# Optimization experiments

Hardware: AMD Instinct MI355X
Metric: run time of the kernel (lower is better)

The kernel has to match this reference:

```python
import jax, jax.numpy as jnp
import numpy as np

EMBED_DIM = 512

def setup_inputs() -> dict:
    key = jax.random.key(0)
    ks = jax.random.split(key, 8)
    B, N, M, C = 4, 4096, 4096, EMBED_DIM
    s = 1.0 / np.sqrt(C)
    return {
        "rgb_features": jax.random.normal(ks[0], (B, N, C), jnp.float32),
        "depth_features": jax.random.normal(ks[1], (B, M, C), jnp.float32),
        "Wq": jax.random.normal(ks[2], (C, C), jnp.float32) * s,
        "bq": jnp.zeros((C,), jnp.float32),
        "Wk": jax.random.normal(ks[3], (C, C), jnp.float32) * s,
        "bk": jnp.zeros((C,), jnp.float32),
        "Wv": jax.random.normal(ks[4], (C, C), jnp.float32) * s,
        "bv": jnp.zeros((C,), jnp.float32),
    }

def reference(rgb_features, depth_features, Wq, bq, Wk, bk, Wv, bv):
    C = rgb_features.shape[-1]
    scale = C ** (-0.5)
    Q = rgb_features @ Wq + bq          # [B, N, C]
    K = depth_features @ Wk + bk        # [B, M, C]
    V = depth_features @ Wv + bv        # [B, M, C]
    scores = jnp.einsum('bnc,bmc->bnm', Q, K) * scale
    attn = jax.nn.softmax(scores, axis=-1)
    return jnp.einsum('bnm,bmc->bnc', attn, V)
```

## Files before the change

kernel.cpp:

```cpp
#include <hip/hip_runtime.h>
#include <hip/hip_bf16.h>
#include <stdint.h>


typedef unsigned short u16;
typedef __attribute__((ext_vector_type(8))) short bf16x8;
typedef __attribute__((ext_vector_type(16))) float f32x16;
typedef __attribute__((ext_vector_type(4))) unsigned short u16x4;

#define GLD_LDS16(g, l)                                                        \
  __builtin_amdgcn_global_load_lds(                                            \
      (const __attribute__((address_space(1))) unsigned int*)(g),              \
      (__attribute__((address_space(3))) unsigned int*)(l), 16, 0, 0)

__device__ __forceinline__ u16 f2bf(float f) {
  unsigned x = __float_as_uint(f);
  return (u16)((x + 0x7fffu + ((x >> 16) & 1u)) >> 16);
}
__device__ __forceinline__ float bf2f(short s) {
  return __uint_as_float((unsigned)(unsigned short)s << 16);
}

template <int TM, int TN, int WC, int BIAS_MODE, bool OUT_F32, int MINW>
__global__ __launch_bounds__(256, MINW) void gemm32(
    const u16* __restrict__ A, const u16* __restrict__ Bm,
    const float* __restrict__ bias, void* __restrict__ Cv, int M, int N, int K,
    long long sAb, long long sBb, long long sCb) {
  constexpr int WROWS = TM * WC / 4;
  constexpr int WCOLS = TN / WC;
  constexpr int MSUB = WROWS / 32;
  constexpr int NSUB = WCOLS / 32;
  constexpr int CA = TM / 64;
  constexpr int CB = TN / 64;

  const int bz = blockIdx.z;
  A += (size_t)bz * sAb;
  Bm += (size_t)bz * sBb;

  const int bm = blockIdx.y * TM;
  const int bn = blockIdx.x * TN;

  __shared__ u16 As[TM * 32];
  __shared__ u16 Bs[TN * 32];

  const int tid = threadIdx.x;
  const int wave = tid >> 6;
  const int lane = tid & 63;
  const int ln31 = lane & 31;
  const int half = lane >> 5;
  const int wr = wave / WC;
  const int wc = wave % WC;

  const int rowA = lane >> 2;
  const int swz = ((lane & 3) ^ ((rowA + (rowA >> 2)) & 3)) * 8;
  const int gl = (ln31 + (ln31 >> 2)) & 3;

  f32x16 acc[MSUB][NSUB] = {};

  for (int k0 = 0; k0 < K; k0 += 32) {
    __syncthreads();
#pragma unroll
    for (int r = 0; r < CA; ++r) {
      const int ch = wave * CA + r;
      GLD_LDS16(A + (size_t)(bm + ch * 16 + rowA) * K + k0 + swz,
                As + ch * 16 * 32);
    }
#pragma unroll
    for (int r = 0; r < CB; ++r) {
      const int ch = wave * CB + r;
      GLD_LDS16(Bm + (size_t)(bn + ch * 16 + rowA) * K + k0 + swz,
                Bs + ch * 16 * 32);
    }
    __syncthreads();

#pragma unroll
    for (int kc = 0; kc < 2; ++kc) {
      const int p = ((kc * 2 + half) ^ gl) * 8;
      bf16x8 af[MSUB], bfv[NSUB];
#pragma unroll
      for (int mt = 0; mt < MSUB; ++mt)
        af[mt] = *(const bf16x8*)&As[(wr * WROWS + mt * 32 + ln31) * 32 + p];
#pragma unroll
      for (int nt = 0; nt < NSUB; ++nt)
        bfv[nt] = *(const bf16x8*)&Bs[(wc * WCOLS + nt * 32 + ln31) * 32 + p];
#pragma unroll
      for (int mt = 0; mt < MSUB; ++mt)
#pragma unroll
        for (int nt = 0; nt < NSUB; ++nt)
          acc[mt][nt] = __builtin_amdgcn_mfma_f32_32x32x16_bf16(
              af[mt], bfv[nt], acc[mt][nt], 0, 0, 0);
    }
  }

  const int crow0 = bm + wr * WROWS + 4 * half;
  const int ccol0 = bn + wc * WCOLS + ln31;
#pragma unroll
  for (int mt = 0; mt < MSUB; ++mt) {
#pragma unroll
    for (int nt = 0; nt < NSUB; ++nt) {
      const int col = ccol0 + nt * 32;
#pragma unroll
      for (int r = 0; r < 16; ++r) {
        const int row = crow0 + mt * 32 + (r & 3) + 8 * (r >> 2);
        float v = acc[mt][nt][r];
        if constexpr (BIAS_MODE == 1) v += bias[col];
        if constexpr (BIAS_MODE == 2) v += bias[row];
        const size_t idx = (size_t)bz * (size_t)sCb + (size_t)row * N + col;
        if constexpr (OUT_F32)
          ((float*)Cv)[idx] = v;
        else
          ((u16*)Cv)[idx] = f2bf(v);
      }
    }
  }
}

__global__ __launch_bounds__(512, 2) void sexp_gemm(
    const u16* __restrict__ Q, const u16* __restrict__ Kb,
    u16* __restrict__ S, float scale) {
  const int bz = blockIdx.z;
  const u16* A = Q + (size_t)bz * (4096ull * 512ull);
  const u16* B = Kb + (size_t)bz * (4096ull * 512ull);
  u16* Sb = S + (size_t)bz * (4096ull * 4096ull);

  const int bm = blockIdx.y * 256;
  const int bn = blockIdx.x * 128;

  __shared__ u16 As[2][256 * 32];
  __shared__ u16 Bs[2][128 * 32];

  const int tid = threadIdx.x;
  const int wave = tid >> 6;
  const int lane = tid & 63;
  const int ln31 = lane & 31;
  const int half = lane >> 5;
  const int wr = wave >> 1;
  const int wc = wave & 1;

  const int rowA = lane >> 2;
  const int swz = ((lane & 3) ^ ((rowA + (rowA >> 2)) & 3)) * 8;
  const int gl = (ln31 + (ln31 >> 2)) & 3;

  f32x16 acc[2][2] = {};

  auto stage = [&](int buf, int k0) {
#pragma unroll
    for (int r = 0; r < 2; ++r) {
      const int ch = wave * 2 + r;
      GLD_LDS16(A + (size_t)(bm + ch * 16 + rowA) * 512 + k0 + swz,
                As[buf] + ch * 16 * 32);
    }
    GLD_LDS16(B + (size_t)(bn + wave * 16 + rowA) * 512 + k0 + swz,
              Bs[buf] + wave * 16 * 32);
  };

  stage(0, 0);
  for (int it = 0; it < 16; ++it) {
    __syncthreads();
    if (it + 1 < 16) stage((it + 1) & 1, (it + 1) * 32);
    const int buf = it & 1;
#pragma unroll
    for (int kc = 0; kc < 2; ++kc) {
      const int p = ((kc * 2 + half) ^ gl) * 8;
      bf16x8 af[2], bfv[2];
#pragma unroll
      for (int mt = 0; mt < 2; ++mt)
        af[mt] = *(const bf16x8*)&As[buf][(wr * 64 + mt * 32 + ln31) * 32 + p];
#pragma unroll
      for (int nt = 0; nt < 2; ++nt)
        bfv[nt] = *(const bf16x8*)&Bs[buf][(wc * 64 + nt * 32 + ln31) * 32 + p];
#pragma unroll
      for (int mt = 0; mt < 2; ++mt)
#pragma unroll
        for (int nt = 0; nt < 2; ++nt)
          acc[mt][nt] = __builtin_amdgcn_mfma_f32_32x32x16_bf16(
              af[mt], bfv[nt], acc[mt][nt], 0, 0, 0);
    }
  }

  const int crow0 = bm + wr * 64 + 4 * half;
  const int ccol0 = bn + wc * 64 + ln31;
#pragma unroll
  for (int mt = 0; mt < 2; ++mt) {
#pragma unroll
    for (int nt = 0; nt < 2; ++nt) {
      const int col = ccol0 + nt * 32;
#pragma unroll
      for (int r = 0; r < 16; ++r) {
        const int row = crow0 + mt * 32 + (r & 3) + 8 * (r >> 2);
        Sb[(size_t)row * 4096 + col] = f2bf(__expf(acc[mt][nt][r] * scale));
      }
    }
  }
}

__global__ __launch_bounds__(512, 2) void pv_gemm(
    const u16* __restrict__ P, const u16* __restrict__ Vt,
    float* __restrict__ O) {
  const int bz = blockIdx.z;
  const u16* A = P + (size_t)bz * (4096ull * 4096ull);
  const u16* B = Vt + (size_t)bz * (512ull * 4096ull);
  float* Ob = O + (size_t)bz * (4096ull * 512ull);

  const int bm = blockIdx.y * 64;

  __shared__ u16 As[64 * 32];
  __shared__ u16 Bs[512 * 32];
  __shared__ float den_s[64];

  const int tid = threadIdx.x;
  const int wave = tid >> 6;
  const int lane = tid & 63;
  const int ln31 = lane & 31;
  const int half = lane >> 5;

  const int rowA = lane >> 2;
  const int swz = ((lane & 3) ^ ((rowA + (rowA >> 2)) & 3)) * 8;
  const int gl = (ln31 + (ln31 >> 2)) & 3;

  f32x16 acc[2][2] = {};
  float rsum[2] = {0.f, 0.f};

  for (int k0 = 0; k0 < 4096; k0 += 32) {
    __syncthreads();
    if (wave < 4)
      GLD_LDS16(A + (size_t)(bm + wave * 16 + rowA) * 4096 + k0 + swz,
                As + wave * 16 * 32);
#pragma unroll
    for (int r = 0; r < 4; ++r) {
      const int ch = wave * 4 + r;
      GLD_LDS16(B + (size_t)(ch * 16 + rowA) * 4096 + k0 + swz,
                Bs + ch * 16 * 32);
    }
    __syncthreads();

#pragma unroll
    for (int kc = 0; kc < 2; ++kc) {
      const int p = ((kc * 2 + half) ^ gl) * 8;
      bf16x8 af[2], bfv[2];
#pragma unroll
      for (int mt = 0; mt < 2; ++mt)
        af[mt] = *(const bf16x8*)&As[(mt * 32 + ln31) * 32 + p];
#pragma unroll
      for (int nt = 0; nt < 2; ++nt)
        bfv[nt] = *(const bf16x8*)&Bs[(wave * 64 + nt * 32 + ln31) * 32 + p];
#pragma unroll
      for (int mt = 0; mt < 2; ++mt) {
#pragma unroll
        for (int j = 0; j < 8; ++j) rsum[mt] += bf2f(af[mt][j]);
#pragma unroll
        for (int nt = 0; nt < 2; ++nt)
          acc[mt][nt] = __builtin_amdgcn_mfma_f32_32x32x16_bf16(
              af[mt], bfv[nt], acc[mt][nt], 0, 0, 0);
      }
    }
  }

#pragma unroll
  for (int mt = 0; mt < 2; ++mt) rsum[mt] += __shfl_xor(rsum[mt], 32, 64);
  __syncthreads();
  if (wave == 0 && half == 0) {
    den_s[ln31] = rsum[0];
    den_s[32 + ln31] = rsum[1];
  }
  __syncthreads();

  const int crow0 = 4 * half;
  const int ccol0 = wave * 64 + ln31;
#pragma unroll
  for (int mt = 0; mt < 2; ++mt) {
#pragma unroll
    for (int r = 0; r < 16; ++r) {
      const int rl = crow0 + mt * 32 + (r & 3) + 8 * (r >> 2);
      const float rd = 1.0f / den_s[rl];
#pragma unroll
      for (int nt = 0; nt < 2; ++nt)
        Ob[(size_t)(bm + rl) * 512 + ccol0 + nt * 32] = acc[mt][nt][r] * rd;
    }
  }
}

__global__ __launch_bounds__(256) void cvt_pair(const float* __restrict__ x,
                                                const float* __restrict__ y,
                                                u16* __restrict__ ox,
                                                u16* __restrict__ oy, int n4) {
  const int i = blockIdx.x * 256 + threadIdx.x;
  if (i >= n4) return;
  const float4 a = ((const float4*)x)[i];
  const float4 b = ((const float4*)y)[i];
  u16x4 oa, ob;
  oa[0] = f2bf(a.x); oa[1] = f2bf(a.y); oa[2] = f2bf(a.z); oa[3] = f2bf(a.w);
  ob[0] = f2bf(b.x); ob[1] = f2bf(b.y); ob[2] = f2bf(b.z); ob[3] = f2bf(b.w);
  ((u16x4*)ox)[i] = oa;
  ((u16x4*)oy)[i] = ob;
}

__global__ __launch_bounds__(256) void wtrans_k(const float* __restrict__ W,
                                                u16* __restrict__ WT) {
  const int tr = blockIdx.y * 64;
  const int tc = blockIdx.x * 64;
  __shared__ float T[64][65];
  const int t = threadIdx.x;
  const int r0 = t >> 4;
  const int c0 = (t & 15) * 4;
#pragma unroll
  for (int rr = 0; rr < 4; ++rr) {
    const int row = rr * 16 + r0;
    const float4 w = *(const float4*)&W[(size_t)(tr + row) * 512 + tc + c0];
    T[row][c0 + 0] = w.x; T[row][c0 + 1] = w.y;
    T[row][c0 + 2] = w.z; T[row][c0 + 3] = w.w;
  }
  __syncthreads();
#pragma unroll
  for (int rr = 0; rr < 4; ++rr) {
    const int orow = rr * 16 + r0;
    u16x4 o;
#pragma unroll
    for (int j = 0; j < 4; ++j) o[j] = f2bf(T[c0 + j][orow]);
    *(u16x4*)&WT[(size_t)(tc + orow) * 512 + tr + c0] = o;
  }
}

extern "C" void kernel_launch(void* const* d_in, const int* in_sizes, int n_in,
                              void* d_out, int out_size, void* d_ws,
                              size_t ws_size, hipStream_t stream) {
  const float* rgb = (const float*)d_in[0];
  const float* dep = (const float*)d_in[1];
  const float* Wq = (const float*)d_in[2];
  const float* bq = (const float*)d_in[3];
  const float* Wk = (const float*)d_in[4];
  const float* bk = (const float*)d_in[5];
  const float* Wv = (const float*)d_in[6];
  const float* bv = (const float*)d_in[7];
  float* out = (float*)d_out;

  const int B = 4, N = 4096, M = 4096, C = 512;
  const size_t nBNC = (size_t)B * N * C;
  const float scale = 0.044194173824159216f;

  char* ws = (char*)d_ws;
  size_t off = 0;
  auto carve = [&](size_t bytes) -> void* {
    void* p = ws + off;
    off += (bytes + 255) & ~(size_t)255;
    return p;
  };
  u16* rgb_bf = (u16*)carve(nBNC * 2);
  u16* dep_bf = (u16*)carve(nBNC * 2);
  u16* WqT = (u16*)carve((size_t)C * C * 2);
  u16* WkT = (u16*)carve((size_t)C * C * 2);
  u16* WvT = (u16*)carve((size_t)C * C * 2);
  u16* Qb = (u16*)carve(nBNC * 2);
  u16* Kb = (u16*)carve(nBNC * 2);
  u16* Vt = (u16*)carve(nBNC * 2);
  u16* Sb = (u16*)carve((size_t)B * N * M * 2);

  const long long strQ = (long long)N * C;
  const long long strV = (long long)C * M;

  cvt_pair<<<8192, 256, 0, stream>>>(rgb, dep, rgb_bf, dep_bf, (int)(nBNC / 4));
  wtrans_k<<<dim3(8, 8), 256, 0, stream>>>(Wq, WqT);
  wtrans_k<<<dim3(8, 8), 256, 0, stream>>>(Wk, WkT);
  wtrans_k<<<dim3(8, 8), 256, 0, stream>>>(Wv, WvT);

  gemm32<128, 128, 2, 1, false, 4><<<dim3(4, 128, 1), 256, 0, stream>>>(
      rgb_bf, WqT, bq, Qb, 16384, 512, 512, 0, 0, 0);
  gemm32<128, 128, 2, 1, false, 4><<<dim3(4, 128, 1), 256, 0, stream>>>(
      dep_bf, WkT, bk, Kb, 16384, 512, 512, 0, 0, 0);
  gemm32<128, 128, 2, 2, false, 4><<<dim3(32, 4, 4), 256, 0, stream>>>(
      WvT, dep_bf, bv, Vt, 512, 4096, 512, 0, strQ, strV);

  sexp_gemm<<<dim3(32, 16, 4), 512, 0, stream>>>(Qb, Kb, Sb, scale);

  pv_gemm<<<dim3(1, 64, 4), 512, 0, stream>>>(Sb, Vt, out);
}
```

Before: 412.7 us.

## Double-buffer all GEMMs, unify score-exp kernel, split PV GEMM across output columns

Folds the separate exp-scores kernel into the generic gemm32 template and gives that template double-buffered LDS staging, so every projection GEMM overlaps global-to-LDS loads with MFMA work. The score GEMM now runs with 128x128 tiles and 256 threads instead of 256x128 tiles and 512 threads. The PV GEMM is split into two 256-column halves with 256-thread blocks and double buffering. This doubles the grid for more parallelism, but each half re-reads the P matrix and recomputes the row sums.

```diff
diff --git a/kernel.cpp b/kernel.cpp
--- a/kernel.cpp
+++ b/kernel.cpp
@@ -21,13 +21,13 @@
   return __uint_as_float((unsigned)(unsigned short)s << 16);
 }
 
-template <int TM, int TN, int WC, int BIAS_MODE, bool OUT_F32, int MINW>
+template <int TM, int TN, int BIAS_MODE, int OUT_MODE, int MINW>
 __global__ __launch_bounds__(256, MINW) void gemm32(
     const u16* __restrict__ A, const u16* __restrict__ Bm,
     const float* __restrict__ bias, void* __restrict__ Cv, int M, int N, int K,
-    long long sAb, long long sBb, long long sCb) {
-  constexpr int WROWS = TM * WC / 4;
-  constexpr int WCOLS = TN / WC;
+    long long sAb, long long sBb, long long sCb, float scale) {
+  constexpr int WROWS = TM / 2;
+  constexpr int WCOLS = TN / 2;
   constexpr int MSUB = WROWS / 32;
   constexpr int NSUB = WCOLS / 32;
   constexpr int CA = TM / 64;
@@ -40,94 +40,8 @@
   const int bm = blockIdx.y * TM;
   const int bn = blockIdx.x * TN;
 
-  __shared__ u16 As[TM * 32];
-  __shared__ u16 Bs[TN * 32];
-
-  const int tid = threadIdx.x;
-  const int wave = tid >> 6;
-  const int lane = tid & 63;
-  const int ln31 = lane & 31;
-  const int half = lane >> 5;
-  const int wr = wave / WC;
-  const int wc = wave % WC;
-
-  const int rowA = lane >> 2;
-  const int swz = ((lane & 3) ^ ((rowA + (rowA >> 2)) & 3)) * 8;
-  const int gl = (ln31 + (ln31 >> 2)) & 3;
-
-  f32x16 acc[MSUB][NSUB] = {};
-
-  for (int k0 = 0; k0 < K; k0 += 32) {
-    __syncthreads();
-#pragma unroll
-    for (int r = 0; r < CA; ++r) {
-      const int ch = wave * CA + r;
-      GLD_LDS16(A + (size_t)(bm + ch * 16 + rowA) * K + k0 + swz,
-                As + ch * 16 * 32);
-    }
-#pragma unroll
-    for (int r = 0; r < CB; ++r) {
-      const int ch = wave * CB + r;
-      GLD_LDS16(Bm + (size_t)(bn + ch * 16 + rowA) * K + k0 + swz,
-                Bs + ch * 16 * 32);
-    }
-    __syncthreads();
-
-#pragma unroll
-    for (int kc = 0; kc < 2; ++kc) {
-      const int p = ((kc * 2 + half) ^ gl) * 8;
-      bf16x8 af[MSUB], bfv[NSUB];
-#pragma unroll
-      for (int mt = 0; mt < MSUB; ++mt)
-        af[mt] = *(const bf16x8*)&As[(wr * WROWS + mt * 32 + ln31) * 32 + p];
-#pragma unroll
-      for (int nt = 0; nt < NSUB; ++nt)
-        bfv[nt] = *(const bf16x8*)&Bs[(wc * WCOLS + nt * 32 + ln31) * 32 + p];
-#pragma unroll
-      for (int mt = 0; mt < MSUB; ++mt)
-#pragma unroll
-        for (int nt = 0; nt < NSUB; ++nt)
-          acc[mt][nt] = __builtin_amdgcn_mfma_f32_32x32x16_bf16(
-              af[mt], bfv[nt], acc[mt][nt], 0, 0, 0);
-    }
-  }
-
-  const int crow0 = bm + wr * WROWS + 4 * half;
-  const int ccol0 = bn + wc * WCOLS + ln31;
-#pragma unroll
-  for (int mt = 0; mt < MSUB; ++mt) {
-#pragma unroll
-    for (int nt = 0; nt < NSUB; ++nt) {
-      const int col = ccol0 + nt * 32;
-#pragma unroll
-      for (int r = 0; r < 16; ++r) {
-        const int row = crow0 + mt * 32 + (r & 3) + 8 * (r >> 2);
-        float v = acc[mt][nt][r];
-        if constexpr (BIAS_MODE == 1) v += bias[col];
-        if constexpr (BIAS_MODE == 2) v += bias[row];
-        const size_t idx = (size_t)bz * (size_t)sCb + (size_t)row * N + col;
-        if constexpr (OUT_F32)
-          ((float*)Cv)[idx] = v;
-        else
-          ((u16*)Cv)[idx] = f2bf(v);
-      }
-    }
-  }
-}
-
-__global__ __launch_bounds__(512, 2) void sexp_gemm(
-    const u16* __restrict__ Q, const u16* __restrict__ Kb,
-    u16* __restrict__ S, float scale) {
-  const int bz = blockIdx.z;
-  const u16* A = Q + (size_t)bz * (4096ull * 512ull);
-  const u16* B = Kb + (size_t)bz * (4096ull * 512ull);
-  u16* Sb = S + (size_t)bz * (4096ull * 4096ull);
-
-  const int bm = blockIdx.y * 256;
-  const int bn = blockIdx.x * 128;
-
-  __shared__ u16 As[2][256 * 32];
-  __shared__ u16 Bs[2][128 * 32];
+  __shared__ u16 As[2][TM * 32];
+  __shared__ u16 Bs[2][TN * 32];
 
   const int tid = threadIdx.x;
   const int wave = tid >> 6;
@@ -141,60 +55,76 @@
   const int swz = ((lane & 3) ^ ((rowA + (rowA >> 2)) & 3)) * 8;
   const int gl = (ln31 + (ln31 >> 2)) & 3;
 
-  f32x16 acc[2][2] = {};
+  f32x16 acc[MSUB][NSUB] = {};
 
   auto stage = [&](int buf, int k0) {
 #pragma unroll
-    for (int r = 0; r < 2; ++r) {
-      const int ch = wave * 2 + r;
-      GLD_LDS16(A + (size_t)(bm + ch * 16 + rowA) * 512 + k0 + swz,
+    for (int r = 0; r < CA; ++r) {
+      const int ch = wave * CA + r;
+      GLD_LDS16(A + (size_t)(bm + ch * 16 + rowA) * K + k0 + swz,
                 As[buf] + ch * 16 * 32);
     }
-    GLD_LDS16(B + (size_t)(bn + wave * 16 + rowA) * 512 + k0 + swz,
-              Bs[buf] + wave * 16 * 32);
+#pragma unroll
+    for (int r = 0; r < CB; ++r) {
+      const int ch = wave * CB + r;
+      GLD_LDS16(Bm + (size_t)(bn + ch * 16 + rowA) * K + k0 + swz,
+                Bs[buf] + ch * 16 * 32);
+    }
   };
 
+  const int niter = K >> 5;
   stage(0, 0);
-  for (int it = 0; it < 16; ++it) {
+  for (int it = 0; it < niter; ++it) {
     __syncthreads();
-    if (it + 1 < 16) stage((it + 1) & 1, (it + 1) * 32);
+    if (it + 1 < niter) stage((it + 1) & 1, (it + 1) * 32);
     const int buf = it & 1;
 #pragma unroll
     for (int kc = 0; kc < 2; ++kc) {
       const int p = ((kc * 2 + half) ^ gl) * 8;
-      bf16x8 af[2], bfv[2];
-#pragma unroll
-      for (int mt = 0; mt < 2; ++mt)
-        af[mt] = *(const bf16x8*)&As[buf][(wr * 64 + mt * 32 + ln31) * 32 + p];
-#pragma unroll
-      for (int nt = 0; nt < 2; ++nt)
-        bfv[nt] = *(const bf16x8*)&Bs[buf][(wc * 64 + nt * 32 + ln31) * 32 + p];
-#pragma unroll
-      for (int mt = 0; mt < 2; ++mt)
-#pragma unroll
-        for (int nt = 0; nt < 2; ++nt)
+      bf16x8 af[MSUB], bfv[NSUB];
+#pragma unroll
+      for (int mt = 0; mt < MSUB; ++mt)
+        af[mt] =
+            *(const bf16x8*)&As[buf][(wr * WROWS + mt * 32 + ln31) * 32 + p];
+#pragma unroll
+      for (int nt = 0; nt < NSUB; ++nt)
+        bfv[nt] =
+            *(const bf16x8*)&Bs[buf][(wc * WCOLS + nt * 32 + ln31) * 32 + p];
+#pragma unroll
+      for (int mt = 0; mt < MSUB; ++mt)
+#pragma unroll
+        for (int nt = 0; nt < NSUB; ++nt)
           acc[mt][nt] = __builtin_amdgcn_mfma_f32_32x32x16_bf16(
               af[mt], bfv[nt], acc[mt][nt], 0, 0, 0);
     }
   }
 
-  const int crow0 = bm + wr * 64 + 4 * half;
-  const int ccol0 = bn + wc * 64 + ln31;
-#pragma unroll
-  for (int mt = 0; mt < 2; ++mt) {
-#pragma unroll
-    for (int nt = 0; nt < 2; ++nt) {
+  const int crow0 = bm + wr * WROWS + 4 * half;
+  const int ccol0 = bn + wc * WCOLS + ln31;
+#pragma unroll
+  for (int mt = 0; mt < MSUB; ++mt) {
+#pragma unroll
+    for (int nt = 0; nt < NSUB; ++nt) {
       const int col = ccol0 + nt * 32;
 #pragma unroll
       for (int r = 0; r < 16; ++r) {
         const int row = crow0 + mt * 32 + (r & 3) + 8 * (r >> 2);
-        Sb[(size_t)row * 4096 + col] = f2bf(__expf(acc[mt][nt][r] * scale));
+        float v = acc[mt][nt][r];
+        if constexpr (BIAS_MODE == 1) v += bias[col];
+        if constexpr (BIAS_MODE == 2) v += bias[row];
+        const size_t idx = (size_t)bz * (size_t)sCb + (size_t)row * N + col;
+        if constexpr (OUT_MODE == 0)
+          ((u16*)Cv)[idx] = f2bf(v);
+        else if constexpr (OUT_MODE == 1)
+          ((float*)Cv)[idx] = v;
+        else
+          ((u16*)Cv)[idx] = f2bf(__expf(v * scale));
       }
     }
   }
 }
 
-__global__ __launch_bounds__(512, 2) void pv_gemm(
+__global__ __launch_bounds__(256, 2) void pv_gemm(
     const u16* __restrict__ P, const u16* __restrict__ Vt,
     float* __restrict__ O) {
   const int bz = blockIdx.z;
@@ -203,9 +133,10 @@
   float* Ob = O + (size_t)bz * (4096ull * 512ull);
 
   const int bm = blockIdx.y * 64;
-
-  __shared__ u16 As[64 * 32];
-  __shared__ u16 Bs[512 * 32];
+  const int bn = blockIdx.x * 256;
+
+  __shared__ u16 As[2][64 * 32];
+  __shared__ u16 Bs[2][256 * 32];
   __shared__ float den_s[64];
 
   const int tid = threadIdx.x;
@@ -221,29 +152,33 @@
   f32x16 acc[2][2] = {};
   float rsum[2] = {0.f, 0.f};
 
-  for (int k0 = 0; k0 < 4096; k0 += 32) {
-    __syncthreads();
-    if (wave < 4)
-      GLD_LDS16(A + (size_t)(bm + wave * 16 + rowA) * 4096 + k0 + swz,
-                As + wave * 16 * 32);
+  auto stage = [&](int buf, int k0) {
+    GLD_LDS16(A + (size_t)(bm + wave * 16 + rowA) * 4096 + k0 + swz,
+              As[buf] + wave * 16 * 32);
 #pragma unroll
     for (int r = 0; r < 4; ++r) {
       const int ch = wave * 4 + r;
-      GLD_LDS16(B + (size_t)(ch * 16 + rowA) * 4096 + k0 + swz,
-                Bs + ch * 16 * 32);
-    }
+      GLD_LDS16(B + (size_t)(bn + ch * 16 + rowA) * 4096 + k0 + swz,
+                Bs[buf] + ch * 16 * 32);
+    }
+  };
+
+  stage(0, 0);
+  for (int it = 0; it < 128; ++it) {
     __syncthreads();
-
+    if (it + 1 < 128) stage((it + 1) & 1, (it + 1) * 32);
+    const int buf = it & 1;
 #pragma unroll
     for (int kc = 0; kc < 2; ++kc) {
       const int p = ((kc * 2 + half) ^ gl) * 8;
       bf16x8 af[2], bfv[2];
 #pragma unroll
       for (int mt = 0; mt < 2; ++mt)
-        af[mt] = *(const bf16x8*)&As[(mt * 32 + ln31) * 32 + p];
+        af[mt] = *(const bf16x8*)&As[buf][(mt * 32 + ln31) * 32 + p];
 #pragma unroll
       for (int nt = 0; nt < 2; ++nt)
-        bfv[nt] = *(const bf16x8*)&Bs[(wave * 64 + nt * 32 + ln31) * 32 + p];
+        bfv[nt] =
+            *(const bf16x8*)&Bs[buf][(wave * 64 + nt * 32 + ln31) * 32 + p];
 #pragma unroll
       for (int mt = 0; mt < 2; ++mt) {
 #pragma unroll
@@ -266,7 +201,7 @@
   __syncthreads();
 
   const int crow0 = 4 * half;
-  const int ccol0 = wave * 64 + ln31;
+  const int ccol0 = bn + wave * 64 + ln31;
 #pragma unroll
   for (int mt = 0; mt < 2; ++mt) {
 #pragma unroll
@@ -356,6 +291,7 @@
   u16* Sb = (u16*)carve((size_t)B * N * M * 2);
 
   const long long strQ = (long long)N * C;
+  const long long strS = (long long)N * M;
   const long long strV = (long long)C * M;
 
   cvt_pair<<<8192, 256, 0, stream>>>(rgb, dep, rgb_bf, dep_bf, (int)(nBNC / 4));
@@ -363,14 +299,15 @@
   wtrans_k<<<dim3(8, 8), 256, 0, stream>>>(Wk, WkT);
   wtrans_k<<<dim3(8, 8), 256, 0, stream>>>(Wv, WvT);
 
-  gemm32<128, 128, 2, 1, false, 4><<<dim3(4, 128, 1), 256, 0, stream>>>(
-      rgb_bf, WqT, bq, Qb, 16384, 512, 512, 0, 0, 0);
-  gemm32<128, 128, 2, 1, false, 4><<<dim3(4, 128, 1), 256, 0, stream>>>(
-      dep_bf, WkT, bk, Kb, 16384, 512, 512, 0, 0, 0);
-  gemm32<128, 128, 2, 2, false, 4><<<dim3(32, 4, 4), 256, 0, stream>>>(
-      WvT, dep_bf, bv, Vt, 512, 4096, 512, 0, strQ, strV);
-
-  sexp_gemm<<<dim3(32, 16, 4), 512, 0, stream>>>(Qb, Kb, Sb, scale);
-
-  pv_gemm<<<dim3(1, 64, 4), 512, 0, stream>>>(Sb, Vt, out);
-}
+  gemm32<128, 128, 1, 0, 4><<<dim3(4, 128, 1), 256, 0, stream>>>(
+      rgb_bf, WqT, bq, Qb, 16384, 512, 512, 0, 0, 0, 1.f);
+  gemm32<128, 128, 1, 0, 4><<<dim3(4, 128, 1), 256, 0, stream>>>(
+      dep_bf, WkT, bk, Kb, 16384, 512, 512, 0, 0, 0, 1.f);
+  gemm32<128, 128, 2, 0, 4><<<dim3(32, 4, 4), 256, 0, stream>>>(
+      WvT, dep_bf, bv, Vt, 512, 4096, 512, 0, strQ, strV, 1.f);
+
+  gemm32<128, 128, 0, 2, 4><<<dim3(32, 32, 4), 256, 0, stream>>>(
+      Qb, Kb, nullptr, Sb, 4096, 4096, 512, strQ, strQ, strS, scale);
+
+  pv_gemm<<<dim3(2, 64, 4), 256, 0, stream>>>(Sb, Vt, out);
+}
```

Result: faster. 383.5 us (-7.1%).
